# Performance work log

Measured on AMD Instinct MI355X. Metric: run time of the kernel, lower is better.

Reference implementation:

```python
import jax, jax.numpy as jnp
import numpy as np

B, N, C, H = 2, 2048, 256, 8
HD = C // H
LN_EPS = 1e-5
BN_EPS = 1e-5  # eval-mode BatchNorm with running_mean=0, running_var=1


def _ln(x, g, b):
    # LayerNorm over last dim
    m = jnp.mean(x, axis=-1, keepdims=True)
    v = jnp.mean((x - m) ** 2, axis=-1, keepdims=True)
    return (x - m) * jax.lax.rsqrt(v + LN_EPS) * g + b


def _ln_cn(x, g, b):
    # x: [B,C,N], normalize over C (torch does transpose -> LN -> transpose)
    return jnp.swapaxes(_ln(jnp.swapaxes(x, 1, 2), g, b), 1, 2)


def _cdist(a, b):
    # a: [B,N,D], b: [B,M,D] -> [B,N,M] euclidean
    d2 = (jnp.sum(a * a, -1)[:, :, None] + jnp.sum(b * b, -1)[:, None, :]
          - 2.0 * jnp.einsum('bnd,bmd->bnm', a, b))
    return jnp.sqrt(jnp.maximum(d2, 0.0))


def _conv1x1(w, x, b=None):
    # w: [O,C], x: [B,C,N]
    y = jnp.einsum('oc,bcn->bon', w, x)
    return y if b is None else y + b[None, :, None]


def setup_inputs() -> dict:
    key = jax.random.key(0)
    ks = jax.random.split(key, 32)
    s = 0.02
    inp = {
        'xyz_A': jax.random.normal(ks[0], (B, N, 3), jnp.float32),
        'featA': jax.random.normal(ks[1], (B, C, N), jnp.float32),
        'xyz_B': jax.random.normal(ks[2], (B, N, 3), jnp.float32),
        'featB': jax.random.normal(ks[3], (B, C, N), jnp.float32),
        'ln_in_g': jnp.ones((C,), jnp.float32),
        'ln_in_b': jnp.zeros((C,), jnp.float32),
        'Wq': jax.random.normal(ks[4], (C, C), jnp.float32) * s,
        'bq': jnp.zeros((C,), jnp.float32),
        'Wk': jax.random.normal(ks[5], (C, C), jnp.float32) * s,
        'bk': jnp.zeros((C,), jnp.float32),
        'Wv': jax.random.normal(ks[6], (C, C), jnp.float32) * s,
        'bv': jnp.zeros((C,), jnp.float32),
        'sb_w1': jax.random.normal(ks[7], (H // 2, 1), jnp.float32) * s,
        'sb_bn_g': jnp.ones((H // 2,), jnp.float32),
        'sb_bn_b': jnp.zeros((H // 2,), jnp.float32),
        'sb_w2': jax.random.normal(ks[8], (H, H // 2), jnp.float32) * s,
        'sb_b2': jnp.zeros((H,), jnp.float32),
        'Wqd': jax.random.normal(ks[9], (C, C), jnp.float32) * s,
        'bqd': jnp.zeros((C,), jnp.float32),
        'Wkd': jax.random.normal(ks[10], (C, C), jnp.float32) * s,
        'bkd': jnp.zeros((C,), jnp.float32),
        'ln_sim_g': jnp.ones((C,), jnp.float32),
        'ln_sim_b': jnp.zeros((C,), jnp.float32),
        'ln_dis_g': jnp.ones((C,), jnp.float32),
        'ln_dis_b': jnp.zeros((C,), jnp.float32),
        'Wf1': jax.random.normal(ks[11], (2 * C, 3 * C), jnp.float32) * s,
        'bnf_g': jnp.ones((2 * C,), jnp.float32),
        'bnf_b': jnp.zeros((2 * C,), jnp.float32),
        'Wf2': jax.random.normal(ks[12], (C, 2 * C), jnp.float32) * s,
        'bf2': jnp.zeros((C,), jnp.float32),
    }
    return inp


def reference(xyz_A, featA, xyz_B, featB, ln_in_g, ln_in_b, Wq, bq, Wk, bk, Wv, bv,
              sb_w1, sb_bn_g, sb_bn_b, sb_w2, sb_b2, Wqd, bqd, Wkd, bkd,
              ln_sim_g, ln_sim_b, ln_dis_g, ln_dis_b, Wf1, bnf_g, bnf_b, Wf2, bf2):
    featA_norm = _ln_cn(featA, ln_in_g, ln_in_b)  # [B,C,N]

    # spatial bias: cdist -> 1x1 conv2d MLP over channel dim
    dist = _cdist(xyz_A, xyz_B)  # [B,N,N]
    h = jnp.einsum('oi,binm->bonm', sb_w1, -dist[:, None])  # [B,H/2,N,N]
    h = h * (sb_bn_g / np.sqrt(1.0 + BN_EPS))[None, :, None, None] + sb_bn_b[None, :, None, None]
    h = jax.nn.relu(h)
    spatial_bias = jnp.einsum('oi,binm->bonm', sb_w2, h) + sb_b2[None, :, None, None]  # [B,H,N,N]

    # similarity path
    q = _conv1x1(Wq, featA_norm, bq).reshape(B, H, HD, N).transpose(0, 1, 3, 2)  # [B,H,N,hd]
    k = _conv1x1(Wk, featB, bk).reshape(B, H, HD, N).transpose(0, 1, 3, 2)
    sim_scores = jnp.einsum('bhnd,bhmd->bhnm', q, k) / np.sqrt(HD) + spatial_bias

    # dissimilarity path: feature-space cdist
    qd = jnp.swapaxes(_conv1x1(Wqd, featA_norm, bqd), 1, 2)  # [B,N,C]
    kd = jnp.swapaxes(_conv1x1(Wkd, featB, bkd), 1, 2)
    dissim_scores = _cdist(qd, kd)[:, None] + spatial_bias  # [B,H,N,N]

    sim_w = jax.nn.softmax(sim_scores, axis=-1)
    dis_w = jax.nn.softmax(dissim_scores, axis=-1)

    v = _conv1x1(Wv, featB, bv).reshape(B, H, HD, N).transpose(0, 1, 3, 2)  # [B,H,N,hd]
    ctx_sim = jnp.einsum('bhnm,bhmd->bhnd', sim_w, v).transpose(0, 1, 3, 2).reshape(B, C, N)
    ctx_sim = _ln_cn(ctx_sim, ln_sim_g, ln_sim_b)
    ctx_dis = jnp.einsum('bhnm,bhmd->bhnd', dis_w, v).transpose(0, 1, 3, 2).reshape(B, C, N)
    ctx_dis = _ln_cn(ctx_dis, ln_dis_g, ln_dis_b)

    fused_in = jnp.concatenate([featA_norm, ctx_sim, ctx_dis], axis=1)  # [B,3C,N]
    f = jnp.einsum('oc,bcn->bon', Wf1, fused_in)
    f = f * (bnf_g / np.sqrt(1.0 + BN_EPS))[None, :, None] + bnf_b[None, :, None]
    f = jax.nn.relu(f)
    fused = jnp.einsum('oc,bcn->bon', Wf2, f) + bf2[None, :, None]

    return fused + featA  # residual (in_channel == out_channel -> Identity)
```

## Files before the change

kernel.cpp:

```cpp
#include <hip/hip_runtime.h>
#include <math.h>

#define B_ 2
#define N_ 2048
#define C_ 256
#define H_ 8
#define HD_ 32
constexpr float LN_EPS_ = 1e-5f;
constexpr float BN_EPS_ = 1e-5f;
constexpr float LOG2E_ = 1.4426950408889634f;
constexpr float ISDL_ = 0.17677669529663687f * 1.4426950408889634f;

typedef __attribute__((ext_vector_type(8))) short bf16x8;
typedef __attribute__((ext_vector_type(4))) float f32x4;

static __device__ inline ushort f2bf(float x) {
    union { float f; uint u; } c{x};
    uint r = (c.u + 0x7FFF + ((c.u >> 16) & 1)) >> 16;
    return (ushort)r;
}
static __device__ inline float bf2f(ushort u) {
    union { uint i; float f; } c; c.i = ((uint)u) << 16; return c.f;
}
static __device__ inline float lane_bcast(float v, int srclane) {
    return __int_as_float(__builtin_amdgcn_ds_bpermute(srclane * 4, __float_as_int(v)));
}
static __device__ inline uint pack_bf2(float lo, float hi) {
    uint ul = __float_as_uint(lo) + 0x8000u;
    uint uh = __float_as_uint(hi) + 0x8000u;
    return __builtin_amdgcn_perm(uh, ul, 0x07060302u);
}

__global__ __launch_bounds__(256)
void k_wconv(const float* __restrict__ Wq, const float* __restrict__ Wk,
             const float* __restrict__ Wv, const float* __restrict__ Wqd,
             const float* __restrict__ Wkd, const float* __restrict__ Wf1,
             const float* __restrict__ Wf2, ushort* __restrict__ dst)
{
    size_t e0 = ((size_t)blockIdx.x * 256 + threadIdx.x) * 8;
    const float* src = Wq; size_t base = 0;
    if (e0 >= 65536)  { src = Wk;  base = 65536; }
    if (e0 >= 131072) { src = Wv;  base = 131072; }
    if (e0 >= 196608) { src = Wqd; base = 196608; }
    if (e0 >= 262144) { src = Wkd; base = 262144; }
    if (e0 >= 327680) { src = Wf1; base = 327680; }
    if (e0 >= 720896) { src = Wf2; base = 720896; }
    float4 a = *(const float4*)(src + (e0 - base));
    float4 b = *(const float4*)(src + (e0 - base) + 4);
    ushort o[8] = {f2bf(a.x), f2bf(a.y), f2bf(a.z), f2bf(a.w),
                   f2bf(b.x), f2bf(b.y), f2bf(b.z), f2bf(b.w)};
    *(uint4*)(dst + e0) = *(uint4*)o;
}

template<bool DO_LN>
__global__ __launch_bounds__(256)
void k_ln_transpose(const float* __restrict__ x,
                    const float* __restrict__ g,
                    const float* __restrict__ bt,
                    ushort* __restrict__ out, int ld)
{
    __shared__ float tile[C_][65];
    __shared__ float red_s[4][64];
    __shared__ float red_q[4][64];
    __shared__ float ms[64];
    __shared__ float rs[64];

    const int b  = blockIdx.x / (N_ / 64);
    const int n0 = (blockIdx.x % (N_ / 64)) * 64;
    const int tid = threadIdx.x;

    for (int i = 0; i < 64; ++i) {
        int c = i * 4 + (tid >> 6);
        int n = tid & 63;
        tile[c][n] = x[((size_t)b * C_ + c) * N_ + n0 + n];
    }
    __syncthreads();

    float gv = 0.f, bv = 0.f;
    if (DO_LN) { gv = g[tid]; bv = bt[tid]; }

    if (DO_LN) {
        const int nl = tid & 63, part = tid >> 6;
        float s = 0.f, q = 0.f;
        for (int j = 0; j < 64; ++j) {
            float v = tile[part * 64 + j][nl];
            s += v; q += v * v;
        }
        red_s[part][nl] = s; red_q[part][nl] = q;
        __syncthreads();
        if (tid < 64) {
            float ss = red_s[0][tid] + red_s[1][tid] + red_s[2][tid] + red_s[3][tid];
            float qq = red_q[0][tid] + red_q[1][tid] + red_q[2][tid] + red_q[3][tid];
            float mean = ss * (1.0f / C_);
            float var  = qq * (1.0f / C_) - mean * mean;
            ms[tid] = mean;
            rs[tid] = rsqrtf(var + LN_EPS_);
        }
        __syncthreads();
    }

    for (int i = 0; i < 64; ++i) {
        float v = tile[tid][i];
        if (DO_LN) v = (v - ms[i]) * rs[i] * gv + bv;
        out[((size_t)b * N_ + n0 + i) * ld + tid] = f2bf(v);
    }
}

template<int EPI, int OUT>
__global__ __launch_bounds__(256)
void k_gemm_bf(const ushort* __restrict__ A, int lda, size_t sAz,
               const ushort* __restrict__ Bw, int ldb, size_t sBz,
               void* __restrict__ Cout_, int ldc, size_t sCz,
               int K,
               const float* __restrict__ aux1,
               const float* __restrict__ aux2)
{
    const int z = blockIdx.z;
    A  += (size_t)z * sAz;
    Bw += (size_t)z * sBz;

    const int r0 = blockIdx.x * 64;
    const int c0 = blockIdx.y * 64;
    const int tid = threadIdx.x;
    const int w = tid >> 6, lane = tid & 63;
    const int wr = w >> 1, wc = w & 1;
    const int ql = lane & 15, g = lane >> 4;

    __shared__ ushort As[64][40];
    __shared__ ushort Bs[64][40];

    f32x4 acc[2][2] = {};
    const int srow = tid >> 2;
    const int sk   = (tid & 3) * 8;

    for (int k0 = 0; k0 < K; k0 += 32) {
        bf16x8 av = *(const bf16x8*)&A[(size_t)(r0 + srow) * lda + k0 + sk];
        bf16x8 bv = *(const bf16x8*)&Bw[(size_t)(c0 + srow) * ldb + k0 + sk];
        __syncthreads();
        *(bf16x8*)&As[srow][sk] = av;
        *(bf16x8*)&Bs[srow][sk] = bv;
        __syncthreads();
        bf16x8 af[2], bf[2];
        #pragma unroll
        for (int i = 0; i < 2; ++i) {
            af[i] = *(const bf16x8*)&As[wr * 32 + i * 16 + ql][8 * g];
            bf[i] = *(const bf16x8*)&Bs[wc * 32 + i * 16 + ql][8 * g];
        }
        #pragma unroll
        for (int mi = 0; mi < 2; ++mi)
            #pragma unroll
            for (int ni = 0; ni < 2; ++ni)
                acc[mi][ni] = __builtin_amdgcn_mfma_f32_16x16x32_bf16(af[mi], bf[ni], acc[mi][ni], 0, 0, 0);
    }

    const float inv_bn = rsqrtf(1.0f + BN_EPS_);
    float*  Cf = (float*)Cout_  + (size_t)z * sCz;
    ushort* Cb = (ushort*)Cout_ + (size_t)z * sCz;
    #pragma unroll
    for (int mi = 0; mi < 2; ++mi) {
        #pragma unroll
        for (int ni = 0; ni < 2; ++ni) {
            #pragma unroll
            for (int r = 0; r < 4; ++r) {
                int row = r0 + wr * 32 + mi * 16 + 4 * g + r;
                int col = c0 + wc * 32 + ni * 16 + ql;
                float v = acc[mi][ni][r];
                if (EPI == 0) {
                    v += aux1[col];
                } else if (EPI == 1) {
                    float qnv = aux1[(size_t)z * N_ + row];
                    float knv = aux2[(size_t)z * N_ + col];
                    v = sqrtf(fmaxf(qnv + knv - 2.0f * v, 0.f));
                } else if (EPI == 2) {
                    v = fmaxf(v * (aux1[col] * inv_bn) + aux2[col], 0.f);
                } else if (EPI == 3) {
                    v += aux1[row];
                }
                if (OUT == 0) Cf[(size_t)row * ldc + col] = v;
                else          Cb[(size_t)row * ldc + col] = f2bf(v);
            }
        }
    }
}

__global__ __launch_bounds__(256)
void k_rownorm(const ushort* __restrict__ x, float* __restrict__ outn)
{
    const int r = blockIdx.x * 4 + (threadIdx.x >> 6);
    const int lane = threadIdx.x & 63;
    uint2 pv = *(const uint2*)&x[(size_t)r * C_ + lane * 4];
    float v0 = bf2f((ushort)(pv.x & 0xffff)), v1 = bf2f((ushort)(pv.x >> 16));
    float v2 = bf2f((ushort)(pv.y & 0xffff)), v3 = bf2f((ushort)(pv.y >> 16));
    float s = v0 * v0 + v1 * v1 + v2 * v2 + v3 * v3;
    #pragma unroll
    for (int off = 32; off; off >>= 1) s += __shfl_xor(s, off);
    if (lane == 0) outn[r] = s;
}

__global__ __launch_bounds__(256)
void k_ln_rows(const float* __restrict__ x, const float* __restrict__ g,
               const float* __restrict__ bt, ushort* __restrict__ outp, int ld)
{
    const int r = blockIdx.x * 4 + (threadIdx.x >> 6);
    const int lane = threadIdx.x & 63;
    float v[4]; float s = 0.f, q = 0.f;
    #pragma unroll
    for (int i = 0; i < 4; ++i) {
        v[i] = x[(size_t)r * C_ + lane + 64 * i];
        s += v[i]; q += v[i] * v[i];
    }
    #pragma unroll
    for (int off = 32; off; off >>= 1) { s += __shfl_xor(s, off); q += __shfl_xor(q, off); }
    float mean = s * (1.0f / C_);
    float var  = q * (1.0f / C_) - mean * mean;
    float rstd = rsqrtf(var + LN_EPS_);
    #pragma unroll
    for (int i = 0; i < 4; ++i) {
        int c = lane + 64 * i;
        outp[(size_t)r * ld + c] = f2bf((v[i] - mean) * rstd * g[c] + bt[c]);
    }
}

__global__ __launch_bounds__(512, 4)
void k_attn5(const ushort* __restrict__ q_bf,
             const ushort* __restrict__ k_bf,
             const ushort* __restrict__ v_c,
             const float* __restrict__ xyzA,
             const float* __restrict__ xyzB,
             const float* __restrict__ cd,
             const float* __restrict__ sb_w1, const float* __restrict__ sb_bn_g,
             const float* __restrict__ sb_bn_b, const float* __restrict__ sb_w2,
             const float* __restrict__ sb_b2,
             ushort* __restrict__ pc,
             float* __restrict__ pml)
{
    __shared__ ushort biasL[4][16][72];
    __shared__ float  cds[16][68];
    __shared__ ushort ps[8][16][72];
    __shared__ float  w2Ls[4][4];
    __shared__ float  b2Ls[4];

    const int n0 = blockIdx.x * 16;
    const int b  = blockIdx.y;
    const int hg   = blockIdx.z & 1;
    const int half = blockIdx.z >> 1;
    const size_t bN = (size_t)b * N_;
    const int tid = threadIdx.x;
    const int w = tid >> 6, lane = tid & 63;
    const int path = w >> 2, hl = w & 3;
    const int h = hg * 4 + hl;
    const int ql = lane & 15, g = lane >> 4;

    if (tid < 4) {
        b2Ls[tid] = sb_b2[hg * 4 + tid] * LOG2E_;
        #pragma unroll
        for (int i = 0; i < 4; ++i) w2Ls[tid][i] = sb_w2[(hg * 4 + tid) * 4 + i] * LOG2E_;
    }

    const float inv_bn = rsqrtf(1.0f + BN_EPS_);
    float w1s_[4], bnb_[4];
    #pragma unroll
    for (int i = 0; i < 4; ++i) {
        w1s_[i] = sb_w1[i] * sb_bn_g[i] * inv_bn;
        bnb_[i] = sb_bn_b[i];
    }

    const int cq = tid >> 5, cm2 = tid & 31;
    const float ax = xyzA[(bN + n0 + cq) * 3 + 0];
    const float ay = xyzA[(bN + n0 + cq) * 3 + 1];
    const float az = xyzA[(bN + n0 + cq) * 3 + 2];

    bf16x8 qfrag = {};
    if (path == 0)
        qfrag = *(const bf16x8*)&q_bf[(bN + n0 + ql) * C_ + h * 32 + 8 * g];

    float m_i = -INFINITY, l_i = 0.f;
    f32x4 ctx0 = {0.f, 0.f, 0.f, 0.f};
    f32x4 ctx1 = {0.f, 0.f, 0.f, 0.f};
    const f32x4 zf = {0.f, 0.f, 0.f, 0.f};

    const int tBeg = half * (N_ / 128);
    const int tEnd = tBeg + (N_ / 128);

    for (int t = tBeg; t < tEnd; ++t) {
        const int m0 = t * 64;
        __syncthreads();

        {
            const int mA = m0 + 2 * cm2;
            const float* pb = xyzB + (bN + mA) * 3;
            float bx0 = pb[0], by0 = pb[1], bz0 = pb[2];
            float bx1 = pb[3], by1 = pb[4], bz1 = pb[5];
            float dx0 = ax - bx0, dy0 = ay - by0, dz0 = az - bz0;
            float dx1 = ax - bx1, dy1 = ay - by1, dz1 = az - bz1;
            float d0 = sqrtf(dx0 * dx0 + dy0 * dy0 + dz0 * dz0);
            float d1 = sqrtf(dx1 * dx1 + dy1 * dy1 + dz1 * dz1);
            float f0[4], f1[4];
            #pragma unroll
            for (int i = 0; i < 4; ++i) {
                f0[i] = fmaxf(fmaf(-w1s_[i], d0, bnb_[i]), 0.f);
                f1[i] = fmaxf(fmaf(-w1s_[i], d1, bnb_[i]), 0.f);
            }
            #pragma unroll
            for (int hh = 0; hh < 4; ++hh) {
                const f32x4 w2v = *(const f32x4*)w2Ls[hh];
                float b0 = b2Ls[hh], b1 = b2Ls[hh];
                #pragma unroll
                for (int i = 0; i < 4; ++i) {
                    b0 = fmaf(w2v[i], f0[i], b0);
                    b1 = fmaf(w2v[i], f1[i], b1);
                }
                *(uint*)&biasL[hh][cq][2 * cm2] = pack_bf2(b0, b1);
            }
            float2 cv = *(const float2*)&cd[(bN + n0 + cq) * (size_t)N_ + mA];
            cds[cq][2 * cm2]     = cv.x * LOG2E_;
            cds[cq][2 * cm2 + 1] = cv.y * LOG2E_;
        }
        __syncthreads();

        bf16x8 af[4];
        if (path == 0) {
            #pragma unroll
            for (int mt = 0; mt < 4; ++mt)
                af[mt] = *(const bf16x8*)&k_bf[(bN + m0 + mt * 16 + ql) * C_ + h * 32 + 8 * g];
        }
        bf16x8 vb[2][2];
        #pragma unroll
        for (int kb = 0; kb < 2; ++kb)
            #pragma unroll
            for (int dt = 0; dt < 2; ++dt)
                vb[kb][dt] = *(const bf16x8*)&v_c[((size_t)b * C_ + h * 32 + dt * 16 + ql) * N_ + m0 + kb * 32 + 8 * g];

        float s[16];
        #pragma unroll
        for (int mt = 0; mt < 4; ++mt) {
            uint2 bw = *(const uint2*)&biasL[hl][ql][16 * mt + 4 * g];
            s[4 * mt + 0] = __uint_as_float(bw.x << 16);
            s[4 * mt + 1] = __uint_as_float(bw.x & 0xffff0000u);
            s[4 * mt + 2] = __uint_as_float(bw.y << 16);
            s[4 * mt + 3] = __uint_as_float(bw.y & 0xffff0000u);
        }

        if (path == 0) {
            #pragma unroll
            for (int mt = 0; mt < 4; ++mt) {
                f32x4 sf = __builtin_amdgcn_mfma_f32_16x16x32_bf16(af[mt], qfrag, zf, 0, 0, 0);
                #pragma unroll
                for (int r = 0; r < 4; ++r)
                    s[4 * mt + r] = fmaf(sf[r], ISDL_, s[4 * mt + r]);
            }
        } else {
            #pragma unroll
            for (int mt = 0; mt < 4; ++mt) {
                f32x4 cv = *(const f32x4*)&cds[ql][16 * mt + 4 * g];
                #pragma unroll
                for (int r = 0; r < 4; ++r)
                    s[4 * mt + r] += cv[r];
            }
        }

        float tmax = s[0];
        #pragma unroll
        for (int j = 1; j < 16; ++j) tmax = fmaxf(tmax, s[j]);
        tmax = fmaxf(tmax, __shfl_xor(tmax, 16));
        tmax = fmaxf(tmax, __shfl_xor(tmax, 32));
        if (!__all(tmax <= m_i + 8.0f)) {
            float mnew = fmaxf(m_i, tmax);
            float scl = exp2f(m_i - mnew);
            l_i *= scl;
            #pragma unroll
            for (int r = 0; r < 4; ++r) {
                float sr = lane_bcast(scl, 4 * g + r);
                ctx0[r] *= sr; ctx1[r] *= sr;
            }
            m_i = mnew;
        }
        float lsum = 0.f;
        #pragma unroll
        for (int j = 0; j < 16; ++j) {
            float pj = exp2f(s[j] - m_i);
            s[j] = pj;
            lsum += pj;
        }
        lsum += __shfl_xor(lsum, 16);
        lsum += __shfl_xor(lsum, 32);
        l_i += lsum;

        #pragma unroll
        for (int mt = 0; mt < 4; ++mt) {
            uint2 pk;
            pk.x = pack_bf2(s[4 * mt + 0], s[4 * mt + 1]);
            pk.y = pack_bf2(s[4 * mt + 2], s[4 * mt + 3]);
            *(uint2*)&ps[w][ql][16 * mt + 4 * g] = pk;
        }

        #pragma unroll
        for (int kb = 0; kb < 2; ++kb) {
            bf16x8 pa = *(const bf16x8*)&ps[w][ql][kb * 32 + 8 * g];
            ctx0 = __builtin_amdgcn_mfma_f32_16x16x32_bf16(pa, vb[kb][0], ctx0, 0, 0, 0);
            ctx1 = __builtin_amdgcn_mfma_f32_16x16x32_bf16(pa, vb[kb][1], ctx1, 0, 0, 0);
        }
    }

    const size_t sl = (size_t)(half * 2 + path) * (B_ * N_);
    #pragma unroll
    for (int r = 0; r < 4; ++r) {
        size_t base = (sl + bN + n0 + 4 * g + r) * C_ + h * 32;
        pc[base + ql]      = f2bf(ctx0[r]);
        pc[base + 16 + ql] = f2bf(ctx1[r]);
    }
    if (g == 0) {
        size_t mlb = ((sl + bN + n0 + ql) * H_ + h) * 2;
        pml[mlb]     = m_i;
        pml[mlb + 1] = l_i;
    }
}

__global__ __launch_bounds__(256)
void k_merge(const ushort* __restrict__ pc, const float* __restrict__ pml,
             float* __restrict__ ctx_sim, float* __restrict__ ctx_dis)
{
    const int row = blockIdx.x;
    const int path = blockIdx.y;
    const int c = threadIdx.x;
    const int h = c >> 5;
    const size_t i0 = (size_t)(0 * 2 + path) * (B_ * N_) + row;
    const size_t i1 = (size_t)(1 * 2 + path) * (B_ * N_) + row;
    const float m0 = pml[(i0 * H_ + h) * 2], l0 = pml[(i0 * H_ + h) * 2 + 1];
    const float m1 = pml[(i1 * H_ + h) * 2], l1 = pml[(i1 * H_ + h) * 2 + 1];
    const float M = fmaxf(m0, m1);
    const float w0 = exp2f(m0 - M), w1 = exp2f(m1 - M);
    const float il = 1.0f / fmaf(l0, w0, l1 * w1);
    const float v0 = bf2f(pc[i0 * C_ + c]);
    const float v1 = bf2f(pc[i1 * C_ + c]);
    float* outp = (path == 0) ? ctx_sim : ctx_dis;
    outp[(size_t)row * C_ + c] = fmaf(v0, w0, v1 * w1) * il;
}

__global__ __launch_bounds__(256)
void k_transpose_add(const float* __restrict__ fused_t,
                     const float* __restrict__ featA,
                     float* __restrict__ out)
{
    __shared__ float t[64][65];
    const int n0 = blockIdx.x * 64, c0 = blockIdx.y * 64, b = blockIdx.z;
    const int tid = threadIdx.x;
    #pragma unroll
    for (int i = 0; i < 16; ++i) {
        int e = i * 256 + tid;
        int nn = e >> 6, cc = e & 63;
        t[nn][cc] = fused_t[((size_t)b * N_ + n0 + nn) * C_ + c0 + cc];
    }
    __syncthreads();
    #pragma unroll
    for (int i = 0; i < 16; ++i) {
        int e = i * 256 + tid;
        int cc = e >> 6, nn = e & 63;
        size_t idx = ((size_t)b * C_ + c0 + cc) * N_ + n0 + nn;
        out[idx] = t[nn][cc] + featA[idx];
    }
}

extern "C" void kernel_launch(void* const* d_in, const int* in_sizes, int n_in,
                              void* d_out, int out_size, void* d_ws, size_t ws_size,
                              hipStream_t stream)
{
    const float* xyz_A   = (const float*)d_in[0];
    const float* featA   = (const float*)d_in[1];
    const float* xyz_B   = (const float*)d_in[2];
    const float* featB   = (const float*)d_in[3];
    const float* ln_in_g = (const float*)d_in[4];
    const float* ln_in_b = (const float*)d_in[5];
    const float* Wq  = (const float*)d_in[6];
    const float* bq  = (const float*)d_in[7];
    const float* Wk  = (const float*)d_in[8];
    const float* bk  = (const float*)d_in[9];
    const float* Wv  = (const float*)d_in[10];
    const float* bv  = (const float*)d_in[11];
    const float* sb_w1   = (const float*)d_in[12];
    const float* sb_bn_g = (const float*)d_in[13];
    const float* sb_bn_b = (const float*)d_in[14];
    const float* sb_w2   = (const float*)d_in[15];
    const float* sb_b2   = (const float*)d_in[16];
    const float* Wqd = (const float*)d_in[17];
    const float* bqd = (const float*)d_in[18];
    const float* Wkd = (const float*)d_in[19];
    const float* bkd = (const float*)d_in[20];
    const float* ln_sim_g = (const float*)d_in[21];
    const float* ln_sim_b = (const float*)d_in[22];
    const float* ln_dis_g = (const float*)d_in[23];
    const float* ln_dis_b = (const float*)d_in[24];
    const float* Wf1   = (const float*)d_in[25];
    const float* bnf_g = (const float*)d_in[26];
    const float* bnf_b = (const float*)d_in[27];
    const float* Wf2   = (const float*)d_in[28];
    const float* bf2   = (const float*)d_in[29];
    float* out = (float*)d_out;

    float* ws = (float*)d_ws;
    size_t off = 0;
    auto alloc = [&](size_t n) { float* p = ws + off; off += n; return p; };
    const size_t RN = (size_t)B_ * N_;

    ushort* fused_bf = (ushort*)alloc(RN * 384);
    ushort* featB_bf = (ushort*)alloc(RN * 128);
    ushort* q_bf     = (ushort*)alloc(RN * 128);
    ushort* k_bf     = (ushort*)alloc(RN * 128);
    ushort* v_bf     = (ushort*)alloc(RN * 128);
    float*  qdkd     = alloc(RN * 256);
    ushort* qd_bf    = (ushort*)qdkd;
    ushort* kd_bf    = qd_bf + RN * C_;
    ushort* wbf      = (ushort*)alloc(425984);
    float*  qn       = alloc(RN);
    float*  kn       = alloc(RN);
    float*  cd       = alloc((size_t)B_ * N_ * N_);
    float*  ctx_dis_t = alloc(RN * C_);
    ushort* pc       = (ushort*)alloc(4 * RN * C_ / 2);
    float*  pml      = alloc(4 * RN * H_ * 2);

    float*  ctx_sim_t = qdkd;
    ushort* fh        = (ushort*)cd;
    float*  fused_t   = cd + RN * 256;

    ushort* wq_bf  = wbf;
    ushort* wk_bf  = wbf + 65536;
    ushort* wv_bf  = wbf + 131072;
    ushort* wqd_bf = wbf + 196608;
    ushort* wkd_bf = wbf + 262144;
    ushort* wf1_bf = wbf + 327680;
    ushort* wf2_bf = wbf + 720896;
    (void)ws_size; (void)in_sizes; (void)n_in; (void)out_size;

    dim3 blk(256);

    k_wconv<<<dim3(416), blk, 0, stream>>>(Wq, Wk, Wv, Wqd, Wkd, Wf1, Wf2, wbf);
    k_ln_transpose<true ><<<dim3(B_ * (N_ / 64)), blk, 0, stream>>>(featA, ln_in_g, ln_in_b, fused_bf, 3 * C_);
    k_ln_transpose<false><<<dim3(B_ * (N_ / 64)), blk, 0, stream>>>(featB, nullptr, nullptr, featB_bf, C_);

    k_gemm_bf<0,1><<<dim3(RN / 64, C_ / 64, 1), blk, 0, stream>>>(fused_bf, 3 * C_, 0, wq_bf,  C_, 0, q_bf,  C_, 0, C_, bq,  nullptr);
    k_gemm_bf<0,1><<<dim3(RN / 64, C_ / 64, 1), blk, 0, stream>>>(featB_bf, C_,     0, wk_bf,  C_, 0, k_bf,  C_, 0, C_, bk,  nullptr);
    k_gemm_bf<3,1><<<dim3(C_ / 64, N_ / 64, B_), blk, 0, stream>>>(wv_bf, C_, 0, featB_bf, C_, (size_t)N_ * C_, v_bf, N_, (size_t)C_ * N_, C_, bv, nullptr);
    k_gemm_bf<0,1><<<dim3(RN / 64, C_ / 64, 1), blk, 0, stream>>>(fused_bf, 3 * C_, 0, wqd_bf, C_, 0, qd_bf, C_, 0, C_, bqd, nullptr);
    k_gemm_bf<0,1><<<dim3(RN / 64, C_ / 64, 1), blk, 0, stream>>>(featB_bf, C_,     0, wkd_bf, C_, 0, kd_bf, C_, 0, C_, bkd, nullptr);

    k_rownorm<<<dim3(RN / 4), blk, 0, stream>>>(qd_bf, qn);
    k_rownorm<<<dim3(RN / 4), blk, 0, stream>>>(kd_bf, kn);
    k_gemm_bf<1,0><<<dim3(N_ / 64, N_ / 64, B_), blk, 0, stream>>>(qd_bf, C_, (size_t)N_ * C_,
                                                                   kd_bf, C_, (size_t)N_ * C_,
                                                                   cd, N_, (size_t)N_ * N_, C_, qn, kn);

    k_attn5<<<dim3(N_ / 16, B_, 4), dim3(512), 0, stream>>>(q_bf, k_bf, v_bf, xyz_A, xyz_B, cd,
                                                            sb_w1, sb_bn_g, sb_bn_b, sb_w2, sb_b2,
                                                            pc, pml);
    k_merge<<<dim3(RN, 2), blk, 0, stream>>>(pc, pml, ctx_sim_t, ctx_dis_t);

    k_ln_rows<<<dim3(RN / 4), blk, 0, stream>>>(ctx_sim_t, ln_sim_g, ln_sim_b, fused_bf + C_,     3 * C_);
    k_ln_rows<<<dim3(RN / 4), blk, 0, stream>>>(ctx_dis_t, ln_dis_g, ln_dis_b, fused_bf + 2 * C_, 3 * C_);

    k_gemm_bf<2,1><<<dim3(RN / 64, (2 * C_) / 64, 1), blk, 0, stream>>>(fused_bf, 3 * C_, 0, wf1_bf, 3 * C_, 0, fh, 2 * C_, 0, 3 * C_, bnf_g, bnf_b);
    k_gemm_bf<0,0><<<dim3(RN / 64, C_ / 64, 1), blk, 0, stream>>>(fh, 2 * C_, 0, wf2_bf, 2 * C_, 0, fused_t, C_, 0, 2 * C_, bf2, nullptr);

    k_transpose_add<<<dim3(N_ / 64, C_ / 64, B_), blk, 0, stream>>>(fused_t, featA, out);
}
```

Baseline: 220.5 us.

## Merge Q/Qd and K/Kd projections, store cdist in bf16, fuse merge with LayerNorm

Reorders the converted weights so the Q and Qd projections, and likewise K and Kd, each run as one wider GEMM into interleaved 512-wide buffers, with bias vectors concatenated by a new small kernel. The feature-space cdist matrix is now written as bf16 rather than fp32, which halves its write and read traffic in the attention kernel. The softmax-partial merge is fused with the post-attention LayerNorm, so the fp32 context intermediates and the two row-LN launches go away. The cost is bf16 rounding on the distance scores before they enter the softmax, which may hurt accuracy.

```diff
diff --git a/kernel.cpp b/kernel.cpp
--- a/kernel.cpp
+++ b/kernel.cpp
@@ -32,17 +32,17 @@
 }
 
 __global__ __launch_bounds__(256)
-void k_wconv(const float* __restrict__ Wq, const float* __restrict__ Wk,
-             const float* __restrict__ Wv, const float* __restrict__ Wqd,
-             const float* __restrict__ Wkd, const float* __restrict__ Wf1,
+void k_wconv(const float* __restrict__ Wq, const float* __restrict__ Wqd,
+             const float* __restrict__ Wk, const float* __restrict__ Wkd,
+             const float* __restrict__ Wv, const float* __restrict__ Wf1,
              const float* __restrict__ Wf2, ushort* __restrict__ dst)
 {
     size_t e0 = ((size_t)blockIdx.x * 256 + threadIdx.x) * 8;
     const float* src = Wq; size_t base = 0;
-    if (e0 >= 65536)  { src = Wk;  base = 65536; }
-    if (e0 >= 131072) { src = Wv;  base = 131072; }
-    if (e0 >= 196608) { src = Wqd; base = 196608; }
-    if (e0 >= 262144) { src = Wkd; base = 262144; }
+    if (e0 >= 65536)  { src = Wqd; base = 65536; }
+    if (e0 >= 131072) { src = Wk;  base = 131072; }
+    if (e0 >= 196608) { src = Wkd; base = 196608; }
+    if (e0 >= 262144) { src = Wv;  base = 262144; }
     if (e0 >= 327680) { src = Wf1; base = 327680; }
     if (e0 >= 720896) { src = Wf2; base = 720896; }
     float4 a = *(const float4*)(src + (e0 - base));
@@ -50,6 +50,16 @@
     ushort o[8] = {f2bf(a.x), f2bf(a.y), f2bf(a.z), f2bf(a.w),
                    f2bf(b.x), f2bf(b.y), f2bf(b.z), f2bf(b.w)};
     *(uint4*)(dst + e0) = *(uint4*)o;
+}
+
+__global__ __launch_bounds__(512)
+void k_bconcat(const float* __restrict__ bq, const float* __restrict__ bqd,
+               const float* __restrict__ bk, const float* __restrict__ bkd,
+               float* __restrict__ bqqd, float* __restrict__ bkkd)
+{
+    int t = threadIdx.x;
+    bqqd[t] = (t < 256) ? bq[t] : bqd[t - 256];
+    bkkd[t] = (t < 256) ? bk[t] : bkd[t - 256];
 }
 
 template<bool DO_LN>
@@ -184,11 +194,11 @@
 }
 
 __global__ __launch_bounds__(256)
-void k_rownorm(const ushort* __restrict__ x, float* __restrict__ outn)
+void k_rownorm(const ushort* __restrict__ x, int ld, float* __restrict__ outn)
 {
     const int r = blockIdx.x * 4 + (threadIdx.x >> 6);
     const int lane = threadIdx.x & 63;
-    uint2 pv = *(const uint2*)&x[(size_t)r * C_ + lane * 4];
+    uint2 pv = *(const uint2*)&x[(size_t)r * ld + lane * 4];
     float v0 = bf2f((ushort)(pv.x & 0xffff)), v1 = bf2f((ushort)(pv.x >> 16));
     float v2 = bf2f((ushort)(pv.y & 0xffff)), v3 = bf2f((ushort)(pv.y >> 16));
     float s = v0 * v0 + v1 * v1 + v2 * v2 + v3 * v3;
@@ -197,37 +207,14 @@
     if (lane == 0) outn[r] = s;
 }
 
-__global__ __launch_bounds__(256)
-void k_ln_rows(const float* __restrict__ x, const float* __restrict__ g,
-               const float* __restrict__ bt, ushort* __restrict__ outp, int ld)
-{
-    const int r = blockIdx.x * 4 + (threadIdx.x >> 6);
-    const int lane = threadIdx.x & 63;
-    float v[4]; float s = 0.f, q = 0.f;
-    #pragma unroll
-    for (int i = 0; i < 4; ++i) {
-        v[i] = x[(size_t)r * C_ + lane + 64 * i];
-        s += v[i]; q += v[i] * v[i];
-    }
-    #pragma unroll
-    for (int off = 32; off; off >>= 1) { s += __shfl_xor(s, off); q += __shfl_xor(q, off); }
-    float mean = s * (1.0f / C_);
-    float var  = q * (1.0f / C_) - mean * mean;
-    float rstd = rsqrtf(var + LN_EPS_);
-    #pragma unroll
-    for (int i = 0; i < 4; ++i) {
-        int c = lane + 64 * i;
-        outp[(size_t)r * ld + c] = f2bf((v[i] - mean) * rstd * g[c] + bt[c]);
-    }
-}
-
+#define QLD_ 512
 __global__ __launch_bounds__(512, 4)
 void k_attn5(const ushort* __restrict__ q_bf,
              const ushort* __restrict__ k_bf,
              const ushort* __restrict__ v_c,
              const float* __restrict__ xyzA,
              const float* __restrict__ xyzB,
-             const float* __restrict__ cd,
+             const ushort* __restrict__ cdb,
              const float* __restrict__ sb_w1, const float* __restrict__ sb_bn_g,
              const float* __restrict__ sb_bn_b, const float* __restrict__ sb_w2,
              const float* __restrict__ sb_b2,
@@ -272,7 +259,7 @@
 
     bf16x8 qfrag = {};
     if (path == 0)
-        qfrag = *(const bf16x8*)&q_bf[(bN + n0 + ql) * C_ + h * 32 + 8 * g];
+        qfrag = *(const bf16x8*)&q_bf[(bN + n0 + ql) * QLD_ + h * 32 + 8 * g];
 
     float m_i = -INFINITY, l_i = 0.f;
     f32x4 ctx0 = {0.f, 0.f, 0.f, 0.f};
@@ -312,9 +299,9 @@
                 }
                 *(uint*)&biasL[hh][cq][2 * cm2] = pack_bf2(b0, b1);
             }
-            float2 cv = *(const float2*)&cd[(bN + n0 + cq) * (size_t)N_ + mA];
-            cds[cq][2 * cm2]     = cv.x * LOG2E_;
-            cds[cq][2 * cm2 + 1] = cv.y * LOG2E_;
+            uint cv = *(const uint*)&cdb[(bN + n0 + cq) * (size_t)N_ + mA];
+            cds[cq][2 * cm2]     = bf2f((ushort)(cv & 0xffff)) * LOG2E_;
+            cds[cq][2 * cm2 + 1] = bf2f((ushort)(cv >> 16)) * LOG2E_;
         }
         __syncthreads();
 
@@ -322,7 +309,7 @@
         if (path == 0) {
             #pragma unroll
             for (int mt = 0; mt < 4; ++mt)
-                af[mt] = *(const bf16x8*)&k_bf[(bN + m0 + mt * 16 + ql) * C_ + h * 32 + 8 * g];
+                af[mt] = *(const bf16x8*)&k_bf[(bN + m0 + mt * 16 + ql) * QLD_ + h * 32 + 8 * g];
         }
         bf16x8 vb[2][2];
         #pragma unroll
@@ -417,9 +404,12 @@
 }
 
 __global__ __launch_bounds__(256)
-void k_merge(const ushort* __restrict__ pc, const float* __restrict__ pml,
-             float* __restrict__ ctx_sim, float* __restrict__ ctx_dis)
-{
+void k_merge_ln(const ushort* __restrict__ pc, const float* __restrict__ pml,
+                const float* __restrict__ g_sim, const float* __restrict__ b_sim,
+                const float* __restrict__ g_dis, const float* __restrict__ b_dis,
+                ushort* __restrict__ fused_bf)
+{
+    __shared__ float rs_[4], rq_[4];
     const int row = blockIdx.x;
     const int path = blockIdx.y;
     const int c = threadIdx.x;
@@ -431,10 +421,23 @@
     const float M = fmaxf(m0, m1);
     const float w0 = exp2f(m0 - M), w1 = exp2f(m1 - M);
     const float il = 1.0f / fmaf(l0, w0, l1 * w1);
-    const float v0 = bf2f(pc[i0 * C_ + c]);
-    const float v1 = bf2f(pc[i1 * C_ + c]);
-    float* outp = (path == 0) ? ctx_sim : ctx_dis;
-    outp[(size_t)row * C_ + c] = fmaf(v0, w0, v1 * w1) * il;
+    const float v = fmaf(bf2f(pc[i0 * C_ + c]), w0, bf2f(pc[i1 * C_ + c]) * w1) * il;
+
+    float s = v, q = v * v;
+    #pragma unroll
+    for (int off = 32; off; off >>= 1) { s += __shfl_xor(s, off); q += __shfl_xor(q, off); }
+    const int wv = c >> 6, lane = c & 63;
+    if (lane == 0) { rs_[wv] = s; rq_[wv] = q; }
+    __syncthreads();
+    float ss = rs_[0] + rs_[1] + rs_[2] + rs_[3];
+    float qq = rq_[0] + rq_[1] + rq_[2] + rq_[3];
+    float mean = ss * (1.0f / C_);
+    float var  = qq * (1.0f / C_) - mean * mean;
+    float rstd = rsqrtf(var + LN_EPS_);
+    const float* gp = path ? g_dis : g_sim;
+    const float* bp = path ? b_dis : b_sim;
+    fused_bf[(size_t)row * (3 * C_) + C_ + path * C_ + c] =
+        f2bf((v - mean) * rstd * gp[c] + bp[c]);
 }
 
 __global__ __launch_bounds__(256)
@@ -504,58 +507,53 @@
 
     ushort* fused_bf = (ushort*)alloc(RN * 384);
     ushort* featB_bf = (ushort*)alloc(RN * 128);
-    ushort* q_bf     = (ushort*)alloc(RN * 128);
-    ushort* k_bf     = (ushort*)alloc(RN * 128);
+    ushort* qqd_bf   = (ushort*)alloc(RN * 256);
+    ushort* kkd_bf   = (ushort*)alloc(RN * 256);
     ushort* v_bf     = (ushort*)alloc(RN * 128);
-    float*  qdkd     = alloc(RN * 256);
-    ushort* qd_bf    = (ushort*)qdkd;
-    ushort* kd_bf    = qd_bf + RN * C_;
     ushort* wbf      = (ushort*)alloc(425984);
+    float*  bqqd     = alloc(512);
+    float*  bkkd     = alloc(512);
     float*  qn       = alloc(RN);
     float*  kn       = alloc(RN);
-    float*  cd       = alloc((size_t)B_ * N_ * N_);
-    float*  ctx_dis_t = alloc(RN * C_);
+    ushort* cd_bf    = (ushort*)alloc((size_t)B_ * N_ * N_ / 2);
     ushort* pc       = (ushort*)alloc(4 * RN * C_ / 2);
     float*  pml      = alloc(4 * RN * H_ * 2);
 
-    float*  ctx_sim_t = qdkd;
-    ushort* fh        = (ushort*)cd;
-    float*  fused_t   = cd + RN * 256;
-
-    ushort* wq_bf  = wbf;
-    ushort* wk_bf  = wbf + 65536;
-    ushort* wv_bf  = wbf + 131072;
-    ushort* wqd_bf = wbf + 196608;
-    ushort* wkd_bf = wbf + 262144;
-    ushort* wf1_bf = wbf + 327680;
-    ushort* wf2_bf = wbf + 720896;
+    ushort* q_bf  = qqd_bf;
+    ushort* qd_bf = qqd_bf + 256;
+    ushort* k_bf  = kkd_bf;
+    ushort* kd_bf = kkd_bf + 256;
+    ushort* fh      = cd_bf;
+    float*  fused_t = (float*)(cd_bf + (size_t)RN * 512);
+
+    ushort* wqqd_bf = wbf;
+    ushort* wkkd_bf = wbf + 131072;
+    ushort* wv_bf   = wbf + 262144;
+    ushort* wf1_bf  = wbf + 327680;
+    ushort* wf2_bf  = wbf + 720896;
     (void)ws_size; (void)in_sizes; (void)n_in; (void)out_size;
 
     dim3 blk(256);
 
-    k_wconv<<<dim3(416), blk, 0, stream>>>(Wq, Wk, Wv, Wqd, Wkd, Wf1, Wf2, wbf);
+    k_wconv<<<dim3(416), blk, 0, stream>>>(Wq, Wqd, Wk, Wkd, Wv, Wf1, Wf2, wbf);
+    k_bconcat<<<dim3(1), dim3(512), 0, stream>>>(bq, bqd, bk, bkd, bqqd, bkkd);
     k_ln_transpose<true ><<<dim3(B_ * (N_ / 64)), blk, 0, stream>>>(featA, ln_in_g, ln_in_b, fused_bf, 3 * C_);
     k_ln_transpose<false><<<dim3(B_ * (N_ / 64)), blk, 0, stream>>>(featB, nullptr, nullptr, featB_bf, C_);
 
-    k_gemm_bf<0,1><<<dim3(RN / 64, C_ / 64, 1), blk, 0, stream>>>(fused_bf, 3 * C_, 0, wq_bf,  C_, 0, q_bf,  C_, 0, C_, bq,  nullptr);
-    k_gemm_bf<0,1><<<dim3(RN / 64, C_ / 64, 1), blk, 0, stream>>>(featB_bf, C_,     0, wk_bf,  C_, 0, k_bf,  C_, 0, C_, bk,  nullptr);
+    k_gemm_bf<0,1><<<dim3(RN / 64, 8, 1), blk, 0, stream>>>(fused_bf, 3 * C_, 0, wqqd_bf, C_, 0, qqd_bf, 512, 0, C_, bqqd, nullptr);
+    k_gemm_bf<0,1><<<dim3(RN / 64, 8, 1), blk, 0, stream>>>(featB_bf, C_,     0, wkkd_bf, C_, 0, kkd_bf, 512, 0, C_, bkkd, nullptr);
     k_gemm_bf<3,1><<<dim3(C_ / 64, N_ / 64, B_), blk, 0, stream>>>(wv_bf, C_, 0, featB_bf, C_, (size_t)N_ * C_, v_bf, N_, (size_t)C_ * N_, C_, bv, nullptr);
-    k_gemm_bf<0,1><<<dim3(RN / 64, C_ / 64, 1), blk, 0, stream>>>(fused_bf, 3 * C_, 0, wqd_bf, C_, 0, qd_bf, C_, 0, C_, bqd, nullptr);
-    k_gemm_bf<0,1><<<dim3(RN / 64, C_ / 64, 1), blk, 0, stream>>>(featB_bf, C_,     0, wkd_bf, C_, 0, kd_bf, C_, 0, C_, bkd, nullptr);
-
-    k_rownorm<<<dim3(RN / 4), blk, 0, stream>>>(qd_bf, qn);
-    k_rownorm<<<dim3(RN / 4), blk, 0, stream>>>(kd_bf, kn);
-    k_gemm_bf<1,0><<<dim3(N_ / 64, N_ / 64, B_), blk, 0, stream>>>(qd_bf, C_, (size_t)N_ * C_,
-                                                                   kd_bf, C_, (size_t)N_ * C_,
-                                                                   cd, N_, (size_t)N_ * N_, C_, qn, kn);
-
-    k_attn5<<<dim3(N_ / 16, B_, 4), dim3(512), 0, stream>>>(q_bf, k_bf, v_bf, xyz_A, xyz_B, cd,
+
+    k_rownorm<<<dim3(RN / 4), blk, 0, stream>>>(qd_bf, 512, qn);
+    k_rownorm<<<dim3(RN / 4), blk, 0, stream>>>(kd_bf, 512, kn);
+    k_gemm_bf<1,1><<<dim3(N_ / 64, N_ / 64, B_), blk, 0, stream>>>(qd_bf, 512, (size_t)N_ * 512,
+                                                                   kd_bf, 512, (size_t)N_ * 512,
+                                                                   cd_bf, N_, (size_t)N_ * N_, C_, qn, kn);
+
+    k_attn5<<<dim3(N_ / 16, B_, 4), dim3(512), 0, stream>>>(q_bf, k_bf, v_bf, xyz_A, xyz_B, cd_bf,
                                                             sb_w1, sb_bn_g, sb_bn_b, sb_w2, sb_b2,
                                                             pc, pml);
-    k_merge<<<dim3(RN, 2), blk, 0, stream>>>(pc, pml, ctx_sim_t, ctx_dis_t);
-
-    k_ln_rows<<<dim3(RN / 4), blk, 0, stream>>>(ctx_sim_t, ln_sim_g, ln_sim_b, fused_bf + C_,     3 * C_);
-    k_ln_rows<<<dim3(RN / 4), blk, 0, stream>>>(ctx_dis_t, ln_dis_g, ln_dis_b, fused_bf + 2 * C_, 3 * C_);
+    k_merge_ln<<<dim3(RN, 2), blk, 0, stream>>>(pc, pml, ln_sim_g, ln_sim_b, ln_dis_g, ln_dis_b, fused_bf);
 
     k_gemm_bf<2,1><<<dim3(RN / 64, (2 * C_) / 64, 1), blk, 0, stream>>>(fused_bf, 3 * C_, 0, wf1_bf, 3 * C_, 0, fh, 2 * C_, 0, 3 * C_, bnf_g, bnf_b);
     k_gemm_bf<0,0><<<dim3(RN / 64, C_ / 64, 1), blk, 0, stream>>>(fh, 2 * C_, 0, wf2_bf, 2 * C_, 0, fused_t, C_, 0, 2 * C_, bf2, nullptr);
```

Result: faster. 206.9 us (-6.2%).
